# Kernel tuning notes

Measured on AMD Instinct MI355X. Metric: run time of the kernel, lower is better.

Reference implementation:

```python
import jax, jax.numpy as jnp
import numpy as np
from jax import lax

P = 16        # patch_size
F = 4         # fourier_freq
E = 8         # num_experts
G = 8         # groupnorm groups = min(8, out_channel)
CIN = 128
COUT = 128
EPS = 1e-5


def conv2d(x, w):
    # x: [B,C,H,W], w: [O,I,kh,kw], stride 1, SAME padding
    return lax.conv_general_dilated(x, w, (1, 1), 'SAME',
                                    dimension_numbers=('NCHW', 'OIHW', 'NCHW'))


def group_norm(x, g, b):
    B, C, H, W = x.shape
    xg = x.reshape(B, G, C // G, H, W)
    m = xg.mean(axis=(2, 3, 4), keepdims=True)
    v = xg.var(axis=(2, 3, 4), keepdims=True)
    xn = ((xg - m) * lax.rsqrt(v + EPS)).reshape(B, C, H, W)
    return xn * g[None, :, None, None] + b[None, :, None, None]


def silu(x):
    return x * jax.nn.sigmoid(x)


def fourier_feats(Hp, Wp):
    # Fourier positional encoding of patch centers -> [Hp, Wp, 4F] (= gate_channel)
    cy = (jnp.arange(Hp, dtype=jnp.float32) + 0.5) / Hp
    cx = (jnp.arange(Wp, dtype=jnp.float32) + 0.5) / Wp
    freqs = (2.0 ** jnp.arange(F, dtype=jnp.float32)) * jnp.pi
    ay = cy[:, None] * freqs[None, :]            # [Hp, F]
    ax = cx[:, None] * freqs[None, :]            # [Wp, F]
    fy = jnp.concatenate([jnp.sin(ay), jnp.cos(ay)], axis=-1)  # [Hp, 2F]
    fx = jnp.concatenate([jnp.sin(ax), jnp.cos(ax)], axis=-1)  # [Wp, 2F]
    return jnp.concatenate([
        jnp.broadcast_to(fy[:, None, :], (Hp, Wp, 2 * F)),
        jnp.broadcast_to(fx[None, :, :], (Hp, Wp, 2 * F)),
    ], axis=-1)


def setup_inputs() -> dict:
    key = jax.random.key(0)
    ks = jax.random.split(key, 5)
    B, H, W = 8, 128, 128
    x = jax.random.normal(ks[0], (B, CIN, H, W), dtype=jnp.float32)
    expert_w = jax.random.normal(ks[1], (E, COUT, CIN, 3, 3), dtype=jnp.float32) * 0.02
    expert_g = jnp.ones((E, COUT), dtype=jnp.float32)
    expert_b = jnp.zeros((E, COUT), dtype=jnp.float32)
    router_w = jax.random.normal(ks[2], (4 * F, E), dtype=jnp.float32) * 0.1
    router_b = jnp.zeros((E,), dtype=jnp.float32)
    merge_g = jnp.ones((COUT,), dtype=jnp.float32)
    merge_b = jnp.zeros((COUT,), dtype=jnp.float32)
    gamma = jnp.ones((1,), dtype=jnp.float32) * 0.01
    post_w = jax.random.normal(ks[3], (COUT, COUT, 3, 3), dtype=jnp.float32) * 0.02
    post_g = jnp.ones((COUT,), dtype=jnp.float32)
    post_b = jnp.zeros((COUT,), dtype=jnp.float32)
    return {'x': x, 'expert_w': expert_w, 'expert_g': expert_g, 'expert_b': expert_b,
            'router_w': router_w, 'router_b': router_b, 'merge_g': merge_g,
            'merge_b': merge_b, 'gamma': gamma, 'post_w': post_w,
            'post_g': post_g, 'post_b': post_b}


def reference(x, expert_w, expert_g, expert_b, router_w, router_b,
              merge_g, merge_b, gamma, post_w, post_g, post_b):
    B, C, H, W = x.shape
    Hp, Wp = H // P, W // P

    # RouterGate: positional Fourier features -> per-patch expert weights
    feats = fourier_feats(Hp, Wp)                       # [Hp, Wp, 4F]
    logits = feats @ router_w + router_b                # [Hp, Wp, E]
    wts = jax.nn.softmax(logits, axis=-1)               # [Hp, Wp, E]

    # ConvExperts: conv3x3 -> GN -> SiLU + residual, vmapped over experts
    def expert(w, g, b):
        return silu(group_norm(conv2d(x, w), g, b)) + x

    outs = jax.vmap(expert)(expert_w, expert_g, expert_b)  # [E, B, C, H, W]

    # Broadcast patch weights to pixel resolution and merge
    wmap = jnp.repeat(jnp.repeat(wts, P, axis=0), P, axis=1)  # [H, W, E]
    merged = jnp.einsum('ebchw,hwe->bchw', outs, wmap)        # [B, C, H, W]

    # merge GN + SiLU, gamma-scaled residual
    y = x + gamma[0] * silu(group_norm(merged, merge_g, merge_b))

    # post block: conv3x3 (no bias) -> GN -> SiLU
    out = silu(group_norm(conv2d(y, post_w), post_g, post_b))
    return out
```

## Files before the change

### kernel.cpp

```cpp
#include <hip/hip_runtime.h>
#include <hip/hip_bf16.h>


typedef __attribute__((ext_vector_type(8))) short bf16x8;
typedef __attribute__((ext_vector_type(4))) float f32x4;
typedef __attribute__((ext_vector_type(2))) float f32x2;
typedef __attribute__((ext_vector_type(8))) unsigned short u16x8;
typedef __attribute__((ext_vector_type(4))) unsigned short u16x4;
typedef __attribute__((ext_vector_type(2))) unsigned int u32x2;
typedef __attribute__((ext_vector_type(2))) int i32x2;
typedef __attribute__((ext_vector_type(2))) long lx2;

__device__ __forceinline__ float b2f(unsigned short u) {
  unsigned int v = ((unsigned int)u) << 16;
  return __builtin_bit_cast(float, v);
}
__device__ __forceinline__ unsigned short f2b(float f) {
  __hip_bfloat16 h = __float2bfloat16(f);
  return __builtin_bit_cast(unsigned short, h);
}
__device__ __forceinline__ float fsilu(float x) {
  float e = __expf(-x);
  return x * __builtin_amdgcn_rcpf(1.f + e);
}
__device__ __forceinline__ void gll16(const void* g, void* l) {
  __builtin_amdgcn_global_load_lds(
      (const __attribute__((address_space(1))) unsigned int*)g,
      (__attribute__((address_space(3))) unsigned int*)l, 16, 0, 0);
}
__device__ __forceinline__ unsigned char f2fp8(float v) {
  return (unsigned char)(__builtin_amdgcn_cvt_pk_fp8_f32(v, v, 0, false) & 0xff);
}

#define PLANE8 8652800ull

__global__ void k_router(const float* __restrict__ rw, const float* __restrict__ rb,
                         float* __restrict__ wts) {
  int t = threadIdx.x;
  if (t >= 64) return;
  int py = t >> 3, px = t & 7;
  float cy = (py + 0.5f) / 8.f, cx = (px + 0.5f) / 8.f;
  const float PI = 3.14159265358979323846f;
  float f[16];
#pragma unroll
  for (int k = 0; k < 4; ++k) {
    float fr = (float)(1 << k) * PI;
    f[k] = sinf(cy * fr); f[4 + k] = cosf(cy * fr);
    f[8 + k] = sinf(cx * fr); f[12 + k] = cosf(cx * fr);
  }
  float lg[8], mx = -1e30f;
#pragma unroll
  for (int e = 0; e < 8; ++e) {
    float a = rb[e];
#pragma unroll
    for (int k = 0; k < 16; ++k) a += f[k] * rw[k * 8 + e];
    lg[e] = a; mx = fmaxf(mx, a);
  }
  float s = 0.f;
#pragma unroll
  for (int e = 0; e < 8; ++e) { lg[e] = __expf(lg[e] - mx); s += lg[e]; }
  float inv = 1.f / s;
#pragma unroll
  for (int e = 0; e < 8; ++e) wts[t * 8 + e] = lg[e] * inv;
}

__global__ void k_zborder(unsigned short* __restrict__ xpu,
                          unsigned char* __restrict__ xp8) {
  int idx = blockIdx.x * 256 + threadIdx.x;
  if (idx >= 8 * 516) return;
  int b = idx / 516, pxi = idx - b * 516;
  int r, c;
  if (pxi < 130)      { r = 0;   c = pxi; }
  else if (pxi < 260) { r = 129; c = pxi - 130; }
  else if (pxi < 388) { r = pxi - 260 + 1; c = 0; }
  else                { r = pxi - 388 + 1; c = 129; }
  size_t pix = (size_t)(b * 130 + r) * 130 + c;
  unsigned short* p = xpu + pix * 128;
#pragma unroll
  for (int j = 0; j < 16; ++j) *(u16x8*)(p + j * 8) = (u16x8)0;
#pragma unroll
  for (int cc = 0; cc < 2; ++cc) {
    f32x4* q = (f32x4*)(xp8 + cc * PLANE8 + pix * 64);
#pragma unroll
    for (int j = 0; j < 4; ++j) q[j] = (f32x4)0.f;
  }
}

__global__ void k_build_xpad(const float* __restrict__ x, __hip_bfloat16* __restrict__ xp,
                             unsigned char* __restrict__ xp8) {
  int bx = blockIdx.x;
  int wb = bx & 1, cib = (bx >> 1) & 1;
  int h = (bx >> 2) & 127, b = bx >> 9;
  int w0 = wb * 64, ci0 = cib * 64;
  __shared__ float t[64][65];
  int tid = threadIdx.x;
#pragma unroll
  for (int r = 0; r < 16; ++r) {
    int idx = r * 256 + tid;
    int i = idx >> 6, j = idx & 63;
    t[i][j] = x[(((size_t)b * 128 + ci0 + i) * 128 + h) * 128 + w0 + j];
  }
  __syncthreads();
  unsigned short* xpu = (unsigned short*)xp;
#pragma unroll
  for (int r = 0; r < 2; ++r) {
    int s = r * 256 + tid;
    int px = s >> 3, cg = s & 7;
    size_t pixbase = ((size_t)b * 130 + h + 1) * 130 + (w0 + px + 1);
    float v[8];
    u16x8 bv;
#pragma unroll
    for (int k = 0; k < 8; ++k) { v[k] = t[cg * 8 + k][px]; bv[k] = f2b(v[k]); }
    int ci = ci0 + cg * 8;
    *(u16x8*)(xpu + pixbase * 128 + ci) = bv;
    int pl = ci >> 6, cl = ci & 63;
    int kg = (cl >> 3) & 3, c = cl >> 5;
    int pk0 = __builtin_amdgcn_cvt_pk_fp8_f32(v[0], v[1], 0, false);
    pk0 = __builtin_amdgcn_cvt_pk_fp8_f32(v[2], v[3], pk0, true);
    int pk1 = __builtin_amdgcn_cvt_pk_fp8_f32(v[4], v[5], 0, false);
    pk1 = __builtin_amdgcn_cvt_pk_fp8_f32(v[6], v[7], pk1, true);
    i32x2 pk = {pk0, pk1};
    *(i32x2*)(xp8 + (size_t)pl * PLANE8 + pixbase * 64 + kg * 16 + c * 8) = pk;
  }
}

__global__ void k_build_w(const float* __restrict__ src, __hip_bfloat16* __restrict__ dst) {
  int o = blockIdx.x * 256 + threadIdx.x;
  if (o >= 147456) return;
  int cl = o & 31, co = (o >> 5) & 127;
  int r9 = o >> 12;
  int tp = r9 % 9, cc = r9 / 9;
  int ci = cc * 32 + cl;
  ((unsigned short*)dst)[o] = f2b(src[((size_t)co * 128 + ci) * 9 + tp]);
}

__global__ void k_build_w8(const float* __restrict__ src, unsigned char* __restrict__ dst) {
  int o = blockIdx.x * 256 + threadIdx.x;
  if (o >= 1179648) return;
  int e = o / 147456;
  int r = o - e * 147456;
  int cc2 = r / 73728;
  int r2 = r - cc2 * 73728;
  int tp = r2 >> 13;
  int r3 = r2 & 8191;
  int co = r3 >> 6, p = r3 & 63;
  int kg = p >> 4, c = (p >> 3) & 1, j = p & 7;
  int ci = cc2 * 64 + c * 32 + kg * 8 + j;
  dst[o] = f2fp8(src[(((size_t)e * 128 + co) * 128 + ci) * 9 + tp]);
}

template <int G>
__global__ __launch_bounds__(512, 2) void k_conv8(
    const unsigned char* __restrict__ xp8, const unsigned char* __restrict__ wt8,
    unsigned char* __restrict__ out8base, float* __restrict__ partials) {
  __shared__ __align__(16) char smem[90112];
  const int cpx = (G * 512) >> 3;
  const int nid = (blockIdx.x & 7) * cpx + (blockIdx.x >> 3);
  const int eg = nid & (G - 1);
  const int t0 = nid / G;
  const int b = t0 >> 6, rp = t0 & 63, h0 = rp * 2;
  const unsigned char* wt = wt8 + (size_t)eg * 147456;
  unsigned char* out8 = out8base + (size_t)eg * 16777216ull;

  const int tid = threadIdx.x;
  const int lane = tid & 63, wid = tid >> 6;
  const int wm = wid >> 1, wn = wid & 1;
  const int rl = lane & 15, kg = lane >> 4;
  const int rowA = wm >> 1;
  const int colA = (wm & 1) * 64;

  int aoff[3][4], boff[3][4];
#pragma unroll
  for (int mb = 0; mb < 4; ++mb) {
    int col = colA + mb * 16 + rl;
#pragma unroll
    for (int kx = 0; kx < 3; ++kx) {
      int px = col + kx;
      aoff[kx][mb] = (rowA * 160 + px) * 64 + (kg ^ ((px >> 1) & 3)) * 16;
    }
  }
#pragma unroll
  for (int kx = 0; kx < 3; ++kx)
#pragma unroll
    for (int nb = 0; nb < 4; ++nb) {
      int co = wn * 64 + nb * 16 + rl;
      boff[kx][nb] = 20480 + ((kx * 128 + co) * 4 + (kg ^ ((co >> 1) & 3))) * 16;
    }

  int soff[6];
  bool isA[6];
#pragma unroll
  for (int it = 0; it < 6; ++it) {
    int s = it * 512 + tid;
    if (s < 1280) {
      int rw = (s >= 640) ? 1 : 0;
      int off = s - rw * 640;
      int px = off >> 2, q = off & 3;
      int qg = q ^ ((px >> 1) & 3);
      isA[it] = true;
      soff[it] = rw * 8320 + px * 64 + qg * 16;
    } else {
      int s2 = s - 1280;
      int tap = s2 >> 9, r3 = s2 & 511;
      int co = r3 >> 2, q = r3 & 3;
      int qg = q ^ ((co >> 1) & 3);
      isA[it] = false;
      soff[it] = tap * 8192 + co * 64 + qg * 16;
    }
  }

  f32x4 acc[4][4] = {};

#define STG8(bi, u)                                                            \
  {                                                                            \
    const int cc2_ = (u) / 3, ky_ = (u) % 3;                                   \
    char* D = smem + (bi) * 45056;                                             \
    const unsigned char* abase =                                               \
        xp8 + (size_t)cc2_ * PLANE8 + (size_t)(b * 130 + h0 + ky_) * 8320;     \
    const unsigned char* bbase = wt + cc2_ * 73728 + ky_ * 24576;              \
    _Pragma("unroll")                                                          \
    for (int it = 0; it < 5; ++it)                                             \
      gll16((isA[it] ? abase : bbase) + soff[it], D + (it * 512 + tid) * 16);  \
    if (tid < 256) gll16(bbase + soff[5], D + (5 * 512 + tid) * 16);           \
  }

  STG8(0, 0);
  for (int u = 0; u < 6; ++u) {
    const int cur = u & 1;
    __syncthreads();
    if (u + 1 < 6) STG8(cur ^ 1, u + 1);
    const char* Al = smem + cur * 45056;
    __builtin_amdgcn_s_setprio(1);
#pragma unroll
    for (int kx = 0; kx < 3; ++kx) {
      lx2 av[4], bv[4];
#pragma unroll
      for (int mb = 0; mb < 4; ++mb) av[mb] = *(const lx2*)(Al + aoff[kx][mb]);
#pragma unroll
      for (int nb = 0; nb < 4; ++nb) bv[nb] = *(const lx2*)(Al + boff[kx][nb]);
#pragma unroll
      for (int c = 0; c < 2; ++c)
#pragma unroll
        for (int mb = 0; mb < 4; ++mb)
#pragma unroll
          for (int nb = 0; nb < 4; ++nb)
            acc[mb][nb] = __builtin_amdgcn_mfma_f32_16x16x32_fp8_fp8(
                bv[nb][c], av[mb][c], acc[mb][nb], 0, 0, 0);
    }
    __builtin_amdgcn_s_setprio(0);
  }
#undef STG8

  float sv[4] = {0, 0, 0, 0}, qv[4] = {0, 0, 0, 0};
#pragma unroll
  for (int mb = 0; mb < 4; ++mb) {
    int px = colA + mb * 16 + rl;
    int h = h0 + rowA, w = px;
    size_t base = (((size_t)b * 128 + h) * 128 + w) * 128;
#pragma unroll
    for (int nb = 0; nb < 4; ++nb) {
      int co0 = wn * 64 + nb * 16 + kg * 4;
      f32x4 v = acc[mb][nb];
#pragma unroll
      for (int j = 0; j < 4; ++j) { sv[nb] += v[j]; qv[nb] += v[j] * v[j]; }
      int pk = __builtin_amdgcn_cvt_pk_fp8_f32(v[0], v[1], 0, false);
      pk = __builtin_amdgcn_cvt_pk_fp8_f32(v[2], v[3], pk, true);
      *(int*)(out8 + base + co0) = pk;
    }
  }
  __syncthreads();
  float* sg = (float*)smem;
  if (tid < 16) sg[tid] = 0.f;
  __syncthreads();
#pragma unroll
  for (int nb = 0; nb < 4; ++nb) {
    float a = sv[nb], q = qv[nb];
#pragma unroll
    for (int o = 32; o > 0; o >>= 1) { a += __shfl_down(a, o); q += __shfl_down(q, o); }
    if (lane == 0) {
      int g = wn * 4 + nb;
      atomicAdd(&sg[g * 2 + 0], a);
      atomicAdd(&sg[g * 2 + 1], q);
    }
  }
  __syncthreads();
  if (tid < 16)
    partials[((size_t)(eg * 8 + b) * 64 + rp) * 16 + tid] = sg[tid];
}

__global__ __launch_bounds__(512, 2) void k_conv(
    const unsigned short* __restrict__ xpu, const unsigned short* __restrict__ wtu,
    unsigned short* __restrict__ outu, float* __restrict__ partials) {
  __shared__ __align__(16) char smem[90112];
  const int nid = (blockIdx.x & 7) * 64 + (blockIdx.x >> 3);
  const int b = nid >> 6, rp = nid & 63, h0 = rp * 2;
  const int tid = threadIdx.x;
  const int lane = tid & 63, wid = tid >> 6;
  const int wm = wid >> 1, wn = wid & 1;
  const int rl = lane & 15, kg = lane >> 4;
  const int rowA = wm >> 1;
  const int colA = (wm & 1) * 64;

  int aoff[3][4], boff[3][4];
#pragma unroll
  for (int mb = 0; mb < 4; ++mb) {
    int col = colA + mb * 16 + rl;
#pragma unroll
    for (int kx = 0; kx < 3; ++kx) {
      int px = col + kx;
      aoff[kx][mb] = (rowA * 160 + px) * 64 + (kg ^ ((px >> 1) & 3)) * 16;
    }
  }
#pragma unroll
  for (int kx = 0; kx < 3; ++kx)
#pragma unroll
    for (int nb = 0; nb < 4; ++nb) {
      int co = wn * 64 + nb * 16 + rl;
      boff[kx][nb] = 20480 + ((kx * 128 + co) * 4 + (kg ^ ((co >> 1) & 3))) * 16;
    }

  int soff[6];
  bool isA[6];
#pragma unroll
  for (int it = 0; it < 6; ++it) {
    int s = it * 512 + tid;
    if (s < 1280) {
      int rw = (s >= 640) ? 1 : 0;
      int off = s - rw * 640;
      int px = off >> 2, q = off & 3;
      int qg = q ^ ((px >> 1) & 3);
      isA[it] = true;
      soff[it] = rw * 33280 + px * 256 + qg * 16;
    } else {
      int s2 = s - 1280;
      int tap = s2 >> 9, r3 = s2 & 511;
      int co = r3 >> 2, q = r3 & 3;
      int qg = q ^ ((co >> 1) & 3);
      isA[it] = false;
      soff[it] = tap * 8192 + co * 64 + qg * 16;
    }
  }

  f32x4 acc[4][4] = {};
  const char* xpb = (const char*)xpu;
  const char* wtb = (const char*)wtu;

#define STAGE(bi, u)                                                           \
  {                                                                            \
    const int cc_ = (u) / 3, ky_ = (u) % 3;                                    \
    char* D = smem + (bi) * 45056;                                             \
    const char* abase =                                                        \
        xpb + (size_t)(b * 130 + h0 + ky_) * 33280 + cc_ * 64;                 \
    const char* bbase = wtb + cc_ * 73728 + ky_ * 24576;                       \
    _Pragma("unroll")                                                          \
    for (int it = 0; it < 5; ++it)                                             \
      gll16((isA[it] ? abase : bbase) + soff[it], D + (it * 512 + tid) * 16);  \
    if (tid < 256) gll16(bbase + soff[5], D + (5 * 512 + tid) * 16);           \
  }

  STAGE(0, 0);
  for (int u = 0; u < 12; ++u) {
    const int cur = u & 1;
    __syncthreads();
    if (u + 1 < 12) STAGE(cur ^ 1, u + 1);
    const char* Al = smem + cur * 45056;
    __builtin_amdgcn_s_setprio(1);
#pragma unroll
    for (int kx = 0; kx < 3; ++kx) {
      bf16x8 aF[4], bF[4];
#pragma unroll
      for (int mb = 0; mb < 4; ++mb) aF[mb] = *(const bf16x8*)(Al + aoff[kx][mb]);
#pragma unroll
      for (int nb = 0; nb < 4; ++nb) bF[nb] = *(const bf16x8*)(Al + boff[kx][nb]);
#pragma unroll
      for (int mb = 0; mb < 4; ++mb)
#pragma unroll
        for (int nb = 0; nb < 4; ++nb)
          acc[mb][nb] = __builtin_amdgcn_mfma_f32_16x16x32_bf16(
              bF[nb], aF[mb], acc[mb][nb], 0, 0, 0);
    }
    __builtin_amdgcn_s_setprio(0);
  }
#undef STAGE

  float sv[4] = {0, 0, 0, 0}, qv[4] = {0, 0, 0, 0};
#pragma unroll
  for (int mb = 0; mb < 4; ++mb) {
    int px = colA + mb * 16 + rl;
    int h = h0 + rowA;
    size_t base = (((size_t)b * 128 + h) * 128 + px) * 128;
#pragma unroll
    for (int nb = 0; nb < 4; ++nb) {
      int co0 = wn * 64 + nb * 16 + kg * 4;
      u16x4 pk;
#pragma unroll
      for (int j = 0; j < 4; ++j) {
        float v = acc[mb][nb][j];
        pk[j] = f2b(v);
        sv[nb] += v; qv[nb] += v * v;
      }
      *(u16x4*)(outu + base + co0) = pk;
    }
  }
  __syncthreads();
  float* sg = (float*)smem;
  if (tid < 16) sg[tid] = 0.f;
  __syncthreads();
#pragma unroll
  for (int nb = 0; nb < 4; ++nb) {
    float a = sv[nb], q = qv[nb];
#pragma unroll
    for (int o = 32; o > 0; o >>= 1) { a += __shfl_down(a, o); q += __shfl_down(q, o); }
    if (lane == 0) {
      int g = wn * 4 + nb;
      atomicAdd(&sg[g * 2 + 0], a);
      atomicAdd(&sg[g * 2 + 1], q);
    }
  }
  __syncthreads();
  if (tid < 16) partials[(size_t)nid * 16 + tid] = sg[tid];
}

__global__ void k_redstats(const float* __restrict__ partials, float* __restrict__ stats,
                           int nper) {
  int set = blockIdx.x;
  const float* p = partials + (size_t)set * 8 * nper * 16;
  float* st = stats + set * 128;
  int t = threadIdx.x;
  int o = t >> 2, j = t & 3;
  int b = o >> 4, slot = o & 15;
  int chunk = nper >> 2;
  float s = 0.f;
  for (int i = j * chunk; i < (j + 1) * chunk; ++i)
    s += p[((size_t)b * nper + i) * 16 + slot];
  s += __shfl_xor(s, 1);
  s += __shfl_xor(s, 2);
  if (j == 0) st[o] = s;
}

__global__ void k_redstats2(const float* __restrict__ p2, float* __restrict__ st) {
  int o = blockIdx.x;
  int b = o >> 4, slot = o & 15;
  float s = 0.f;
  for (int i = threadIdx.x; i < 1024; i += 256)
    s += p2[((size_t)b * 1024 + i) * 16 + slot];
#pragma unroll
  for (int off = 32; off > 0; off >>= 1) s += __shfl_down(s, off);
  __shared__ float wsm[4];
  int lane = threadIdx.x & 63, wv = threadIdx.x >> 6;
  if (lane == 0) wsm[wv] = s;
  __syncthreads();
  if (threadIdx.x == 0) st[o] = wsm[0] + wsm[1] + wsm[2] + wsm[3];
}

template <int NEXP>
__global__ void k_merge(const unsigned char* __restrict__ c0,
                        const unsigned char* __restrict__ c1,
                        const unsigned char* __restrict__ c2,
                        const unsigned char* __restrict__ c3,
                        const float* __restrict__ st, const float* __restrict__ eg,
                        const float* __restrict__ eb, const float* __restrict__ wts,
                        unsigned short* __restrict__ merged,
                        const unsigned short* __restrict__ xp,
                        float* __restrict__ partials2, int e0, int flags) {
  __shared__ float sg[16];
  int tid = threadIdx.x;
  if (tid < 16) sg[tid] = 0.f;
  __syncthreads();
  size_t idx = ((size_t)blockIdx.x * 256 + tid) * 8;
  int co0 = (int)(idx & 127);
  size_t pix = idx >> 7;
  int w = (int)(pix & 127), h = (int)((pix >> 7) & 127), b = (int)(pix >> 14);
  int g = co0 >> 4;
  const float cnt = 16.f * 128.f * 128.f;
  int patch = (h >> 4) * 8 + (w >> 4);
  const unsigned char* cs[4] = {c0, c1, c2, c3};
  float a[8] = {0, 0, 0, 0, 0, 0, 0, 0};
#pragma unroll
  for (int k = 0; k < NEXP; ++k) {
    int e = e0 + k;
    float mean = st[e * 128 + (b * 8 + g) * 2] / cnt;
    float var = st[e * 128 + (b * 8 + g) * 2 + 1] / cnt - mean * mean;
    float rstd = rsqrtf(var + 1e-5f);
    float we = wts[patch * 8 + e];
    f32x4 g0 = *(const f32x4*)(eg + e * 128 + co0);
    f32x4 g1 = *(const f32x4*)(eg + e * 128 + co0 + 4);
    f32x4 b0 = *(const f32x4*)(eb + e * 128 + co0);
    f32x4 b1 = *(const f32x4*)(eb + e * 128 + co0 + 4);
    u32x2 cv = *(const u32x2*)(cs[k] + idx);
    f32x2 d0 = __builtin_amdgcn_cvt_pk_f32_fp8(cv[0], false);
    f32x2 d1 = __builtin_amdgcn_cvt_pk_f32_fp8(cv[0], true);
    f32x2 d2 = __builtin_amdgcn_cvt_pk_f32_fp8(cv[1], false);
    f32x2 d3 = __builtin_amdgcn_cvt_pk_f32_fp8(cv[1], true);
    float d[8] = {d0[0], d0[1], d1[0], d1[1], d2[0], d2[1], d3[0], d3[1]};
#pragma unroll
    for (int i = 0; i < 8; ++i) {
      float gi = (i < 4) ? g0[i] : g1[i - 4];
      float bi = (i < 4) ? b0[i] : b1[i - 4];
      float A = rstd * gi;
      float B = bi - mean * A;
      a[i] += we * fsilu(d[i] * A + B);
    }
  }
  if (flags & 1) {
    u16x8 mv = *(const u16x8*)(merged + idx);
#pragma unroll
    for (int i = 0; i < 8; ++i) a[i] += b2f(mv[i]);
  }
  u16x8 out;
  float s = 0.f, q = 0.f;
  if (flags & 2) {
    const unsigned short* xr =
        xp + (((size_t)b * 130 + h + 1) * 130 + (w + 1)) * 128 + co0;
    u16x8 xv = *(const u16x8*)xr;
#pragma unroll
    for (int i = 0; i < 8; ++i) {
      a[i] += b2f(xv[i]);
      out[i] = f2b(a[i]);
      float rv = b2f(out[i]);
      s += rv; q += rv * rv;
    }
  } else {
#pragma unroll
    for (int i = 0; i < 8; ++i) out[i] = f2b(a[i]);
  }
  *(u16x8*)(merged + idx) = out;
  if (flags & 2) {
    atomicAdd(&sg[g * 2 + 0], s);
    atomicAdd(&sg[g * 2 + 1], q);
    __syncthreads();
    if (tid < 16) partials2[(size_t)blockIdx.x * 16 + tid] = sg[tid];
  }
}

__global__ void k_ypass(const unsigned short* __restrict__ merged,
                        unsigned short* __restrict__ xp,
                        const float* __restrict__ st, const float* __restrict__ mg,
                        const float* __restrict__ mbv, const float* __restrict__ gptr) {
  size_t idx = ((size_t)blockIdx.x * 256 + threadIdx.x) * 8;
  int co0 = (int)(idx & 127);
  size_t pix = idx >> 7;
  int w = (int)(pix & 127), h = (int)((pix >> 7) & 127), b = (int)(pix >> 14);
  int g = co0 >> 4;
  const float cnt = 16.f * 128.f * 128.f;
  float mean = st[(b * 8 + g) * 2] / cnt;
  float var = st[(b * 8 + g) * 2 + 1] / cnt - mean * mean;
  float rstd = rsqrtf(var + 1e-5f);
  float gm = gptr[0];
  unsigned short* xr = xp + (((size_t)b * 130 + h + 1) * 130 + (w + 1)) * 128 + co0;
  u16x8 xv = *(const u16x8*)xr;
  u16x8 mv = *(const u16x8*)(merged + idx);
  u16x8 yv;
#pragma unroll
  for (int i = 0; i < 8; ++i) {
    float xf = b2f(xv[i]);
    float M = b2f(mv[i]);
    float xn = (M - mean) * rstd * mg[co0 + i] + mbv[co0 + i];
    yv[i] = f2b(xf + gm * fsilu(xn));
  }
  *(u16x8*)xr = yv;
}

__global__ void k_final(const __hip_bfloat16* __restrict__ conv, const float* __restrict__ st,
                        const float* __restrict__ pg, const float* __restrict__ pb,
                        float* __restrict__ out) {
  int bx = blockIdx.x;
  int wb = bx & 1, h = (bx >> 1) & 127, b = bx >> 8;
  int w0 = wb * 64;
  __shared__ float t[64][129];
  int tid = threadIdx.x;
  const float cnt = 16.f * 128.f * 128.f;
  const unsigned short* cu = (const unsigned short*)conv;
#pragma unroll
  for (int r = 0; r < 32; ++r) {
    int e2 = r * 256 + tid;
    int co = e2 & 127, wl = e2 >> 7;
    int g = co >> 4;
    float mean = st[(b * 8 + g) * 2] / cnt;
    float var = st[(b * 8 + g) * 2 + 1] / cnt - mean * mean;
    float rstd = rsqrtf(var + 1e-5f);
    float v = b2f(cu[(((size_t)b * 128 + h) * 128 + w0 + wl) * 128 + co]);
    float xn = (v - mean) * rstd * pg[co] + pb[co];
    t[wl][co] = fsilu(xn);
  }
  __syncthreads();
#pragma unroll
  for (int r = 0; r < 8; ++r) {
    int f = r * 256 + tid;
    int jb = f & 15, co = f >> 4;
    f32x4 o;
#pragma unroll
    for (int j = 0; j < 4; ++j) o[j] = t[jb * 4 + j][co];
    *(f32x4*)&out[(((size_t)b * 128 + co) * 128 + h) * 128 + w0 + jb * 4] = o;
  }
}

extern "C" void kernel_launch(void* const* d_in, const int* in_sizes, int n_in,
                              void* d_out, int out_size, void* d_ws, size_t ws_size,
                              hipStream_t stream) {
  const float* x        = (const float*)d_in[0];
  const float* expert_w = (const float*)d_in[1];
  const float* expert_g = (const float*)d_in[2];
  const float* expert_b = (const float*)d_in[3];
  const float* router_w = (const float*)d_in[4];
  const float* router_b = (const float*)d_in[5];
  const float* merge_g  = (const float*)d_in[6];
  const float* merge_b  = (const float*)d_in[7];
  const float* gamma    = (const float*)d_in[8];
  const float* post_w   = (const float*)d_in[9];
  const float* post_g   = (const float*)d_in[10];
  const float* post_b   = (const float*)d_in[11];

  char* ws = (char*)d_ws;
  float* wts            = (float*)(ws + 0);
  float* stats          = (float*)(ws + 2048);
  float* partials       = (float*)(ws + 8192);
  float* partials2      = (float*)(ws + 270336);
  unsigned short* wtbp  = (unsigned short*)(ws + 794624);
  unsigned char* wtb8   = (unsigned char*)(ws + 1089536);
  unsigned short* xpad  = (unsigned short*)(ws + 2269184);
  unsigned char* xpad8  = (unsigned char*)(ws + 36888576);
  const size_t BUFS = 54198272ull;
  const size_t FB = 16777216ull;
  const size_t NEED2 = BUFS + 2 * FB + 33554432ull;
  const size_t NEED4 = BUFS + 4 * FB + 33554432ull;
  int nbuf = (ws_size >= NEED4) ? 4 : 2;
  unsigned char* bufs0 = (unsigned char*)(ws + BUFS);
  unsigned short* merged = (unsigned short*)(ws + BUFS + (size_t)nbuf * FB);
  unsigned short* pbuf = (unsigned short*)(ws + BUFS);
  if (ws_size < NEED2) {
    hipMemsetAsync(d_out, 0, (size_t)out_size * 4, stream);
    return;
  }

  k_zborder<<<17, 256, 0, stream>>>(xpad, xpad8);
  k_router<<<1, 64, 0, stream>>>(router_w, router_b, wts);
  k_build_xpad<<<4096, 256, 0, stream>>>(x, (__hip_bfloat16*)xpad, xpad8);
  k_build_w<<<576, 256, 0, stream>>>(post_w, (__hip_bfloat16*)wtbp);
  k_build_w8<<<4608, 256, 0, stream>>>(expert_w, wtb8);

  if (nbuf == 4) {
    for (int p = 0; p < 2; ++p) {
      k_conv8<4><<<2048, 512, 0, stream>>>(xpad8, wtb8 + (size_t)(p * 4) * 147456,
                                           bufs0, partials);
      k_redstats<<<4, 512, 0, stream>>>(partials, stats + p * 4 * 128, 64);
      int flags = (p > 0 ? 1 : 0) | (p == 1 ? 2 : 0);
      k_merge<4><<<8192, 256, 0, stream>>>(bufs0, bufs0 + FB, bufs0 + 2 * FB,
                                           bufs0 + 3 * FB, stats, expert_g, expert_b,
                                           wts, merged, xpad, partials2, p * 4, flags);
    }
  } else {
    for (int p = 0; p < 4; ++p) {
      k_conv8<2><<<1024, 512, 0, stream>>>(xpad8, wtb8 + (size_t)(p * 2) * 147456,
                                           bufs0, partials);
      k_redstats<<<2, 512, 0, stream>>>(partials, stats + p * 2 * 128, 64);
      int flags = (p > 0 ? 1 : 0) | (p == 3 ? 2 : 0);
      k_merge<2><<<8192, 256, 0, stream>>>(bufs0, bufs0 + FB, bufs0, bufs0 + FB,
                                           stats, expert_g, expert_b, wts, merged,
                                           xpad, partials2, p * 2, flags);
    }
  }
  k_redstats2<<<128, 256, 0, stream>>>(partials2, stats + 8 * 128);
  k_ypass<<<8192, 256, 0, stream>>>(merged, xpad, stats + 8 * 128, merge_g, merge_b, gamma);
  k_conv<<<512, 512, 0, stream>>>(xpad, wtbp, pbuf, partials);
  k_redstats<<<1, 512, 0, stream>>>(partials, stats + 9 * 128, 64);
  k_final<<<2048, 256, 0, stream>>>((const __hip_bfloat16*)pbuf, stats + 9 * 128,
                                    post_g, post_b, (float*)d_out);
}
```

Before: 448.3 us.

## Triple-buffer LDS staging in conv kernels with explicit vmcnt waits

Both conv kernels, fp8 and bf16, move from a double-buffered to a triple-buffered LDS pipeline. Two stages are prefetched up front, and each iteration waits with a partial `s_waitcnt vmcnt(6)` plus a raw barrier instead of a full `__syncthreads`, so loads for stage u+2 overlap compute on stage u. Each stage is padded to 48 KB so that all 512 threads issue six uniform loads with no tid branch; the tail threads duplicate loads into the padding region. The scheduling-priority hints are removed. LDS per block grows to 144 KB, which rules out two resident blocks per CU. The hand-written vmcnt counts must stay correct for the pipeline to be race-free.

```diff
diff --git a/kernel.cpp b/kernel.cpp
--- a/kernel.cpp
+++ b/kernel.cpp
@@ -153,7 +153,7 @@
 __global__ __launch_bounds__(512, 2) void k_conv8(
     const unsigned char* __restrict__ xp8, const unsigned char* __restrict__ wt8,
     unsigned char* __restrict__ out8base, float* __restrict__ partials) {
-  __shared__ __align__(16) char smem[90112];
+  __shared__ __align__(16) char smem[147456];
   const int cpx = (G * 512) >> 3;
   const int nid = (blockIdx.x & 7) * cpx + (blockIdx.x >> 3);
   const int eg = nid & (G - 1);
@@ -187,26 +187,28 @@
       boff[kx][nb] = 20480 + ((kx * 128 + co) * 4 + (kg ^ ((co >> 1) & 3))) * 16;
     }
 
-  int soff[6];
+  int soff[6], loff[6];
   bool isA[6];
 #pragma unroll
   for (int it = 0; it < 6; ++it) {
     int s = it * 512 + tid;
-    if (s < 1280) {
-      int rw = (s >= 640) ? 1 : 0;
-      int off = s - rw * 640;
+    int sc = (s < 2816) ? s : (s - 256);
+    if (sc < 1280) {
+      int rw = (sc >= 640) ? 1 : 0;
+      int off = sc - rw * 640;
       int px = off >> 2, q = off & 3;
       int qg = q ^ ((px >> 1) & 3);
       isA[it] = true;
       soff[it] = rw * 8320 + px * 64 + qg * 16;
     } else {
-      int s2 = s - 1280;
+      int s2 = sc - 1280;
       int tap = s2 >> 9, r3 = s2 & 511;
       int co = r3 >> 2, q = r3 & 3;
       int qg = q ^ ((co >> 1) & 3);
       isA[it] = false;
       soff[it] = tap * 8192 + co * 64 + qg * 16;
     }
+    loff[it] = s * 16;
   }
 
   f32x4 acc[4][4] = {};
@@ -214,23 +216,28 @@
 #define STG8(bi, u)                                                            \
   {                                                                            \
     const int cc2_ = (u) / 3, ky_ = (u) % 3;                                   \
-    char* D = smem + (bi) * 45056;                                             \
+    char* D = smem + (bi) * 49152;                                             \
     const unsigned char* abase =                                               \
         xp8 + (size_t)cc2_ * PLANE8 + (size_t)(b * 130 + h0 + ky_) * 8320;     \
     const unsigned char* bbase = wt + cc2_ * 73728 + ky_ * 24576;              \
     _Pragma("unroll")                                                          \
-    for (int it = 0; it < 5; ++it)                                             \
-      gll16((isA[it] ? abase : bbase) + soff[it], D + (it * 512 + tid) * 16);  \
-    if (tid < 256) gll16(bbase + soff[5], D + (5 * 512 + tid) * 16);           \
+    for (int it = 0; it < 6; ++it)                                             \
+      gll16((isA[it] ? abase : bbase) + soff[it], D + loff[it]);               \
   }
 
   STG8(0, 0);
+  STG8(1, 1);
+#pragma unroll
   for (int u = 0; u < 6; ++u) {
-    const int cur = u & 1;
-    __syncthreads();
-    if (u + 1 < 6) STG8(cur ^ 1, u + 1);
-    const char* Al = smem + cur * 45056;
-    __builtin_amdgcn_s_setprio(1);
+    if (u < 5)
+      asm volatile("s_waitcnt vmcnt(6)" ::: "memory");
+    else
+      asm volatile("s_waitcnt vmcnt(0)" ::: "memory");
+    __builtin_amdgcn_s_barrier();
+    if (u + 2 < 6) {
+      STG8((u + 2) % 3, u + 2);
+    }
+    const char* Al = smem + (u % 3) * 49152;
 #pragma unroll
     for (int kx = 0; kx < 3; ++kx) {
       lx2 av[4], bv[4];
@@ -247,7 +254,6 @@
             acc[mb][nb] = __builtin_amdgcn_mfma_f32_16x16x32_fp8_fp8(
                 bv[nb][c], av[mb][c], acc[mb][nb], 0, 0, 0);
     }
-    __builtin_amdgcn_s_setprio(0);
   }
 #undef STG8
 
@@ -291,7 +297,7 @@
 __global__ __launch_bounds__(512, 2) void k_conv(
     const unsigned short* __restrict__ xpu, const unsigned short* __restrict__ wtu,
     unsigned short* __restrict__ outu, float* __restrict__ partials) {
-  __shared__ __align__(16) char smem[90112];
+  __shared__ __align__(16) char smem[147456];
   const int nid = (blockIdx.x & 7) * 64 + (blockIdx.x >> 3);
   const int b = nid >> 6, rp = nid & 63, h0 = rp * 2;
   const int tid = threadIdx.x;
@@ -319,26 +325,28 @@
       boff[kx][nb] = 20480 + ((kx * 128 + co) * 4 + (kg ^ ((co >> 1) & 3))) * 16;
     }
 
-  int soff[6];
+  int soff[6], loff[6];
   bool isA[6];
 #pragma unroll
   for (int it = 0; it < 6; ++it) {
     int s = it * 512 + tid;
-    if (s < 1280) {
-      int rw = (s >= 640) ? 1 : 0;
-      int off = s - rw * 640;
+    int sc = (s < 2816) ? s : (s - 256);
+    if (sc < 1280) {
+      int rw = (sc >= 640) ? 1 : 0;
+      int off = sc - rw * 640;
       int px = off >> 2, q = off & 3;
       int qg = q ^ ((px >> 1) & 3);
       isA[it] = true;
       soff[it] = rw * 33280 + px * 256 + qg * 16;
     } else {
-      int s2 = s - 1280;
+      int s2 = sc - 1280;
       int tap = s2 >> 9, r3 = s2 & 511;
       int co = r3 >> 2, q = r3 & 3;
       int qg = q ^ ((co >> 1) & 3);
       isA[it] = false;
       soff[it] = tap * 8192 + co * 64 + qg * 16;
     }
+    loff[it] = s * 16;
   }
 
   f32x4 acc[4][4] = {};
@@ -348,23 +356,28 @@
 #define STAGE(bi, u)                                                           \
   {                                                                            \
     const int cc_ = (u) / 3, ky_ = (u) % 3;                                    \
-    char* D = smem + (bi) * 45056;                                             \
+    char* D = smem + (bi) * 49152;                                             \
     const char* abase =                                                        \
         xpb + (size_t)(b * 130 + h0 + ky_) * 33280 + cc_ * 64;                 \
     const char* bbase = wtb + cc_ * 73728 + ky_ * 24576;                       \
     _Pragma("unroll")                                                          \
-    for (int it = 0; it < 5; ++it)                                             \
-      gll16((isA[it] ? abase : bbase) + soff[it], D + (it * 512 + tid) * 16);  \
-    if (tid < 256) gll16(bbase + soff[5], D + (5 * 512 + tid) * 16);           \
+    for (int it = 0; it < 6; ++it)                                             \
+      gll16((isA[it] ? abase : bbase) + soff[it], D + loff[it]);               \
   }
 
   STAGE(0, 0);
+  STAGE(1, 1);
+#pragma unroll
   for (int u = 0; u < 12; ++u) {
-    const int cur = u & 1;
-    __syncthreads();
-    if (u + 1 < 12) STAGE(cur ^ 1, u + 1);
-    const char* Al = smem + cur * 45056;
-    __builtin_amdgcn_s_setprio(1);
+    if (u < 11)
+      asm volatile("s_waitcnt vmcnt(6)" ::: "memory");
+    else
+      asm volatile("s_waitcnt vmcnt(0)" ::: "memory");
+    __builtin_amdgcn_s_barrier();
+    if (u + 2 < 12) {
+      STAGE((u + 2) % 3, u + 2);
+    }
+    const char* Al = smem + (u % 3) * 49152;
 #pragma unroll
     for (int kx = 0; kx < 3; ++kx) {
       bf16x8 aF[4], bF[4];
@@ -379,7 +392,6 @@
           acc[mb][nb] = __builtin_amdgcn_mfma_f32_16x16x32_bf16(
               bF[nb], aF[mb], acc[mb][nb], 0, 0, 0);
     }
-    __builtin_amdgcn_s_setprio(0);
   }
 #undef STAGE
 
```

New measurement: 447.4 us. About the same (-0.2%).

## Use 16x16x128 scaled FP8 MFMA with full-K pixel layout and per-tap pipeline

Applied to the files above, without the earlier changes.

The FP8 expert conv now uses the gfx950 scaled MFMA (K=128) in place of the 16x16x32 fp8 MFMA. This needs a new layout: activations are stored as 128 contiguous channels per padded pixel with an XOR swizzle, and weights are stored per tap as [co][128]. The staging loop changes from 6 stages (channel-half by ky) to 9 taps. Weights are double-buffered per tap and input rows per ky, so MFMA instruction count drops and LDS reads get wider. The change also removes s_setprio from the bf16 post conv and raises LDS use per block, which may limit occupancy.

```diff
diff --git a/kernel.cpp b/kernel.cpp
--- a/kernel.cpp
+++ b/kernel.cpp
@@ -9,7 +9,8 @@
 typedef __attribute__((ext_vector_type(4))) unsigned short u16x4;
 typedef __attribute__((ext_vector_type(2))) unsigned int u32x2;
 typedef __attribute__((ext_vector_type(2))) int i32x2;
-typedef __attribute__((ext_vector_type(2))) long lx2;
+typedef __attribute__((ext_vector_type(4))) int i32x4;
+typedef __attribute__((ext_vector_type(8))) int i32x8;
 
 __device__ __forceinline__ float b2f(unsigned short u) {
   unsigned int v = ((unsigned int)u) << 16;
@@ -31,8 +32,6 @@
 __device__ __forceinline__ unsigned char f2fp8(float v) {
   return (unsigned char)(__builtin_amdgcn_cvt_pk_fp8_f32(v, v, 0, false) & 0xff);
 }
-
-#define PLANE8 8652800ull
 
 __global__ void k_router(const float* __restrict__ rw, const float* __restrict__ rb,
                          float* __restrict__ wts) {
@@ -78,12 +77,9 @@
   unsigned short* p = xpu + pix * 128;
 #pragma unroll
   for (int j = 0; j < 16; ++j) *(u16x8*)(p + j * 8) = (u16x8)0;
-#pragma unroll
-  for (int cc = 0; cc < 2; ++cc) {
-    f32x4* q = (f32x4*)(xp8 + cc * PLANE8 + pix * 64);
-#pragma unroll
-    for (int j = 0; j < 4; ++j) q[j] = (f32x4)0.f;
-  }
+  f32x4* q = (f32x4*)(xp8 + pix * 128);
+#pragma unroll
+  for (int j = 0; j < 8; ++j) q[j] = (f32x4)0.f;
 }
 
 __global__ void k_build_xpad(const float* __restrict__ x, __hip_bfloat16* __restrict__ xp,
@@ -106,21 +102,21 @@
   for (int r = 0; r < 2; ++r) {
     int s = r * 256 + tid;
     int px = s >> 3, cg = s & 7;
-    size_t pixbase = ((size_t)b * 130 + h + 1) * 130 + (w0 + px + 1);
+    int wpad = w0 + px + 1;
+    size_t pixbase = ((size_t)b * 130 + h + 1) * 130 + wpad;
     float v[8];
     u16x8 bv;
 #pragma unroll
     for (int k = 0; k < 8; ++k) { v[k] = t[cg * 8 + k][px]; bv[k] = f2b(v[k]); }
     int ci = ci0 + cg * 8;
     *(u16x8*)(xpu + pixbase * 128 + ci) = bv;
-    int pl = ci >> 6, cl = ci & 63;
-    int kg = (cl >> 3) & 3, c = cl >> 5;
+    int c_phys = (ci >> 4) ^ (wpad & 7);
     int pk0 = __builtin_amdgcn_cvt_pk_fp8_f32(v[0], v[1], 0, false);
     pk0 = __builtin_amdgcn_cvt_pk_fp8_f32(v[2], v[3], pk0, true);
     int pk1 = __builtin_amdgcn_cvt_pk_fp8_f32(v[4], v[5], 0, false);
     pk1 = __builtin_amdgcn_cvt_pk_fp8_f32(v[6], v[7], pk1, true);
     i32x2 pk = {pk0, pk1};
-    *(i32x2*)(xp8 + (size_t)pl * PLANE8 + pixbase * 64 + kg * 16 + c * 8) = pk;
+    *(i32x2*)(xp8 + pixbase * 128 + c_phys * 16 + (ci & 8)) = pk;
   }
 }
 
@@ -139,21 +135,20 @@
   if (o >= 1179648) return;
   int e = o / 147456;
   int r = o - e * 147456;
-  int cc2 = r / 73728;
-  int r2 = r - cc2 * 73728;
-  int tp = r2 >> 13;
-  int r3 = r2 & 8191;
-  int co = r3 >> 6, p = r3 & 63;
-  int kg = p >> 4, c = (p >> 3) & 1, j = p & 7;
-  int ci = cc2 * 64 + c * 32 + kg * 8 + j;
-  dst[o] = f2fp8(src[(((size_t)e * 128 + co) * 128 + ci) * 9 + tp]);
+  int tap = r >> 14;
+  int rr = r & 16383;
+  int co = rr >> 7, byte = rr & 127;
+  int c_phys = byte >> 4, j = byte & 15;
+  int c_log = c_phys ^ (co & 7);
+  int ci = c_log * 16 + j;
+  dst[o] = f2fp8(src[(((size_t)e * 128 + co) * 128 + ci) * 9 + tap]);
 }
 
 template <int G>
 __global__ __launch_bounds__(512, 2) void k_conv8(
     const unsigned char* __restrict__ xp8, const unsigned char* __restrict__ wt8,
     unsigned char* __restrict__ out8base, float* __restrict__ partials) {
-  __shared__ __align__(16) char smem[90112];
+  __shared__ __align__(16) char smem[99328];
   const int cpx = (G * 512) >> 3;
   const int nid = (blockIdx.x & 7) * cpx + (blockIdx.x >> 3);
   const int eg = nid & (G - 1);
@@ -169,94 +164,87 @@
   const int rowA = wm >> 1;
   const int colA = (wm & 1) * 64;
 
-  int aoff[3][4], boff[3][4];
+  int aoff[3][4][2], boff[4][2];
 #pragma unroll
   for (int mb = 0; mb < 4; ++mb) {
     int col = colA + mb * 16 + rl;
 #pragma unroll
     for (int kx = 0; kx < 3; ++kx) {
       int px = col + kx;
-      aoff[kx][mb] = (rowA * 160 + px) * 64 + (kg ^ ((px >> 1) & 3)) * 16;
-    }
-  }
-#pragma unroll
-  for (int kx = 0; kx < 3; ++kx)
+      int base = rowA * 16640 + px * 128;
+      aoff[kx][mb][0] = base + ((2 * kg) ^ (px & 7)) * 16;
+      aoff[kx][mb][1] = base + ((2 * kg + 1) ^ (px & 7)) * 16;
+    }
+  }
+#pragma unroll
+  for (int nb = 0; nb < 4; ++nb) {
+    int co = wn * 64 + nb * 16 + rl;
+    boff[nb][0] = 66560 + co * 128 + ((2 * kg) ^ (co & 7)) * 16;
+    boff[nb][1] = 66560 + co * 128 + ((2 * kg + 1) ^ (co & 7)) * 16;
+  }
+
+  f32x4 acc[4][4] = {};
+
+#define STGA(bi, ky_)                                                          \
+  {                                                                            \
+    const unsigned char* abase =                                               \
+        xp8 + (size_t)(b * 130 + h0 + (ky_)) * 16640;                          \
+    char* D = smem + (bi) * 33280;                                             \
+    _Pragma("unroll")                                                          \
+    for (int it = 0; it < 4; ++it)                                             \
+      gll16(abase + (it * 512 + tid) * 16, D + (it * 512 + tid) * 16);         \
+    if (tid < 32) gll16(abase + (2048 + tid) * 16, D + (2048 + tid) * 16);     \
+  }
+#define STGB(bi, t_)                                                           \
+  {                                                                            \
+    const unsigned char* bbase = wt + (t_) * 16384;                            \
+    char* D = smem + 66560 + (bi) * 16384;                                     \
+    gll16(bbase + tid * 16, D + tid * 16);                                     \
+    gll16(bbase + (512 + tid) * 16, D + (512 + tid) * 16);                     \
+  }
+
+  STGA(0, 0);
+  STGB(0, 0);
+#pragma unroll
+  for (int t = 0; t < 9; ++t) {
+    const int ky = t / 3, kx = t % 3;
+    __syncthreads();
+    if (t + 1 < 9) STGB((t + 1) & 1, t + 1);
+    if (kx == 0 && ky < 2) STGA((ky + 1) & 1, ky + 1);
+    const char* Al = smem + (ky & 1) * 33280;
+    const int bsel = (t & 1) * 16384;
+    i32x8 av[4], bv[4];
+#pragma unroll
+    for (int mb = 0; mb < 4; ++mb) {
+      i32x4 lo = *(const i32x4*)(Al + aoff[kx][mb][0]);
+      i32x4 hi = *(const i32x4*)(Al + aoff[kx][mb][1]);
+      av[mb][0] = lo[0]; av[mb][1] = lo[1]; av[mb][2] = lo[2]; av[mb][3] = lo[3];
+      av[mb][4] = hi[0]; av[mb][5] = hi[1]; av[mb][6] = hi[2]; av[mb][7] = hi[3];
+    }
 #pragma unroll
     for (int nb = 0; nb < 4; ++nb) {
-      int co = wn * 64 + nb * 16 + rl;
-      boff[kx][nb] = 20480 + ((kx * 128 + co) * 4 + (kg ^ ((co >> 1) & 3))) * 16;
-    }
-
-  int soff[6];
-  bool isA[6];
-#pragma unroll
-  for (int it = 0; it < 6; ++it) {
-    int s = it * 512 + tid;
-    if (s < 1280) {
-      int rw = (s >= 640) ? 1 : 0;
-      int off = s - rw * 640;
-      int px = off >> 2, q = off & 3;
-      int qg = q ^ ((px >> 1) & 3);
-      isA[it] = true;
-      soff[it] = rw * 8320 + px * 64 + qg * 16;
-    } else {
-      int s2 = s - 1280;
-      int tap = s2 >> 9, r3 = s2 & 511;
-      int co = r3 >> 2, q = r3 & 3;
-      int qg = q ^ ((co >> 1) & 3);
-      isA[it] = false;
-      soff[it] = tap * 8192 + co * 64 + qg * 16;
-    }
-  }
-
-  f32x4 acc[4][4] = {};
-
-#define STG8(bi, u)                                                            \
-  {                                                                            \
-    const int cc2_ = (u) / 3, ky_ = (u) % 3;                                   \
-    char* D = smem + (bi) * 45056;                                             \
-    const unsigned char* abase =                                               \
-        xp8 + (size_t)cc2_ * PLANE8 + (size_t)(b * 130 + h0 + ky_) * 8320;     \
-    const unsigned char* bbase = wt + cc2_ * 73728 + ky_ * 24576;              \
-    _Pragma("unroll")                                                          \
-    for (int it = 0; it < 5; ++it)                                             \
-      gll16((isA[it] ? abase : bbase) + soff[it], D + (it * 512 + tid) * 16);  \
-    if (tid < 256) gll16(bbase + soff[5], D + (5 * 512 + tid) * 16);           \
-  }
-
-  STG8(0, 0);
-  for (int u = 0; u < 6; ++u) {
-    const int cur = u & 1;
-    __syncthreads();
-    if (u + 1 < 6) STG8(cur ^ 1, u + 1);
-    const char* Al = smem + cur * 45056;
-    __builtin_amdgcn_s_setprio(1);
-#pragma unroll
-    for (int kx = 0; kx < 3; ++kx) {
-      lx2 av[4], bv[4];
-#pragma unroll
-      for (int mb = 0; mb < 4; ++mb) av[mb] = *(const lx2*)(Al + aoff[kx][mb]);
-#pragma unroll
-      for (int nb = 0; nb < 4; ++nb) bv[nb] = *(const lx2*)(Al + boff[kx][nb]);
-#pragma unroll
-      for (int c = 0; c < 2; ++c)
-#pragma unroll
-        for (int mb = 0; mb < 4; ++mb)
-#pragma unroll
-          for (int nb = 0; nb < 4; ++nb)
-            acc[mb][nb] = __builtin_amdgcn_mfma_f32_16x16x32_fp8_fp8(
-                bv[nb][c], av[mb][c], acc[mb][nb], 0, 0, 0);
-    }
-    __builtin_amdgcn_s_setprio(0);
-  }
-#undef STG8
+      i32x4 lo = *(const i32x4*)(smem + bsel + boff[nb][0]);
+      i32x4 hi = *(const i32x4*)(smem + bsel + boff[nb][1]);
+      bv[nb][0] = lo[0]; bv[nb][1] = lo[1]; bv[nb][2] = lo[2]; bv[nb][3] = lo[3];
+      bv[nb][4] = hi[0]; bv[nb][5] = hi[1]; bv[nb][6] = hi[2]; bv[nb][7] = hi[3];
+    }
+#pragma unroll
+    for (int mb = 0; mb < 4; ++mb)
+#pragma unroll
+      for (int nb = 0; nb < 4; ++nb)
+        acc[mb][nb] = __builtin_amdgcn_mfma_scale_f32_16x16x128_f8f6f4(
+            bv[nb], av[mb], acc[mb][nb], 0, 0,
+            0, 0x7F7F7F7F, 0, 0x7F7F7F7F);
+  }
+#undef STGA
+#undef STGB
 
   float sv[4] = {0, 0, 0, 0}, qv[4] = {0, 0, 0, 0};
 #pragma unroll
   for (int mb = 0; mb < 4; ++mb) {
     int px = colA + mb * 16 + rl;
-    int h = h0 + rowA, w = px;
-    size_t base = (((size_t)b * 128 + h) * 128 + w) * 128;
+    int h = h0 + rowA;
+    size_t base = (((size_t)b * 128 + h) * 128 + px) * 128;
 #pragma unroll
     for (int nb = 0; nb < 4; ++nb) {
       int co0 = wn * 64 + nb * 16 + kg * 4;
@@ -364,7 +352,6 @@
     __syncthreads();
     if (u + 1 < 12) STAGE(cur ^ 1, u + 1);
     const char* Al = smem + cur * 45056;
-    __builtin_amdgcn_s_setprio(1);
 #pragma unroll
     for (int kx = 0; kx < 3; ++kx) {
       bf16x8 aF[4], bF[4];
@@ -379,7 +366,6 @@
           acc[mb][nb] = __builtin_amdgcn_mfma_f32_16x16x32_bf16(
               bF[nb], aF[mb], acc[mb][nb], 0, 0, 0);
     }
-    __builtin_amdgcn_s_setprio(0);
   }
 #undef STAGE
 
```

Measured after the change: 396.3 us. -11.6%, faster.
